# Kernel tuning notes

Hardware: AMD Instinct MI355X
Metric: run time of the kernel (lower is better)

## Reference

```python
import jax, jax.numpy as jnp
import numpy as np

B, S, DIN, DOUT, A, T, H = 8, 1024, 1024, 1024, 4, 4, 8  # arity A, T cell types, hidden H


def setup_inputs() -> dict:
    key = jax.random.key(0)
    ks = jax.random.split(key, 6)
    x = jax.random.normal(ks[0], (B, S, DIN), jnp.float32)
    sc = 1.0 / np.sqrt(DIN).astype(np.float32)
    weight = jax.random.uniform(ks[1], (A * DOUT, DIN), jnp.float32, -sc, sc)
    bias = jax.random.uniform(ks[2], (A * DOUT,), jnp.float32, -sc, sc)
    # stacked per-cell-type MLP params: arity -> H -> 1 (tanh)
    cw1 = jax.random.normal(ks[3], (T, A, H), jnp.float32) / np.sqrt(A).astype(np.float32)
    cb1 = jnp.zeros((T, H), jnp.float32)
    cw2 = jax.random.normal(ks[4], (T, H), jnp.float32) / np.sqrt(H).astype(np.float32)
    cb2 = jnp.zeros((T,), jnp.float32)
    return {"x": x, "weight": weight, "bias": bias,
            "cw1": cw1, "cb1": cb1, "cw2": cw2, "cb2": cb2}


def reference(x, weight, bias, cw1, cb1, cw2, cb2):
    T_, A_, H_ = cw1.shape
    Dout = weight.shape[0] // A_
    G = Dout // T_  # neurons per cell type (cell_indices = contiguous blocks via np.repeat)
    # all_inputs = F.linear(input, weight, bias): (B, S, A*Dout)
    z = jnp.einsum('bsd,od->bso', x, weight) + bias
    # slice per-neuron arity chunks -> (B, S, T, G, A)
    z = z.reshape(z.shape[0], z.shape[1], T_, G, A_)
    # per-cell-type MLP applied to every neuron of that type (replaces Python loop)
    h = jnp.tanh(jnp.einsum('bstga,tah->bstgh', z, cw1) + cb1[:, None, :])
    o = jnp.einsum('bstgh,th->bstg', h, cw2) + cb2[:, None]
    # concat over neurons -> (B, S, Dout)
    return o.reshape(o.shape[0], o.shape[1], Dout)
```

## Files before the change

kernel.cpp:

```cpp
#include <hip/hip_runtime.h>


typedef __bf16 bf16x8 __attribute__((ext_vector_type(8)));
typedef float f32x4 __attribute__((ext_vector_type(4)));
typedef float f32x16 __attribute__((ext_vector_type(16)));

#define BM 256
#define BN 128
#define BK 32
#define KDIM 1024
#define NITER (KDIM / BK)
#define ABUF (BM * BK)
#define BUF_ELEMS ((BM + BN) * BK)
#define BUF_BYTES (BUF_ELEMS * 2)
#define ZS 132
#define XN8 (8192 * 1024 / 8)
#define WN8 (4096 * 1024 / 8)

__global__ __launch_bounds__(256) void cvt_bf16_kernel(
    const float* __restrict__ x, const float* __restrict__ w,
    __bf16* __restrict__ xb, __bf16* __restrict__ wb) {
    int i = blockIdx.x * 256 + threadIdx.x;
    const float* src;
    __bf16* dst;
    int j;
    if (i < XN8) { src = x; dst = xb; j = i; }
    else         { src = w; dst = wb; j = i - XN8; }
    const f32x4* p = (const f32x4*)src + 2 * (size_t)j;
    f32x4 a = p[0], b = p[1];
    bf16x8 o;
    o[0] = (__bf16)a[0]; o[1] = (__bf16)a[1]; o[2] = (__bf16)a[2]; o[3] = (__bf16)a[3];
    o[4] = (__bf16)b[0]; o[5] = (__bf16)b[1]; o[6] = (__bf16)b[2]; o[7] = (__bf16)b[3];
    ((bf16x8*)dst)[j] = o;
}

union __align__(16) SmemU {
    __bf16 stg[2 * BUF_ELEMS];
    float  z[64 * ZS];
};

__global__ __launch_bounds__(256, 2) void fused_gemm_mlp_kernel(
    const __bf16* __restrict__ Ag,
    const __bf16* __restrict__ Bg,
    const float* __restrict__ bias,
    const float* __restrict__ cw1,
    const float* __restrict__ cb1,
    const float* __restrict__ cw2,
    const float* __restrict__ cb2,
    float* __restrict__ out)
{
    __shared__ SmemU u;

    const int tid  = threadIdx.x;
    const int wave = tid >> 6;
    const int lane = tid & 63;
    const int wm = wave >> 1;
    const int wn = wave & 1;
    const int bn0 = blockIdx.x * BN;
    const int bm0 = blockIdx.y * BM;

    f32x16 acc[4][2] = {};

    const int srow4 = lane >> 2;
    const int g8    = (((lane & 3) ^ ((lane >> 3) & 3)) * 8);

    const int lr5 = lane & 31;
    const int lk2 = lane >> 5;
    const int sw2 = (lr5 >> 1) & 3;
    const int arow = (wm * 128 + lr5) * (BK * 2);
    const int brow = ABUF * 2 + (wn * 64 + lr5) * (BK * 2);
    int cxo[2];
#pragma unroll
    for (int kh = 0; kh < 2; ++kh)
        cxo[kh] = ((kh * 2 + lk2) ^ sw2) * 16;
    const char* sb = (const char*)u.stg;

    auto stage = [&](int it, int buf) {
        __bf16* dstA = u.stg + buf * BUF_ELEMS;
        __bf16* dstB = dstA + ABUF;
        const int kof = it * BK;
#pragma unroll
        for (int c = 0; c < 4; ++c) {
            const int chunk = wave * 4 + c;
            const __bf16* ga = Ag + (size_t)(bm0 + chunk * 16 + srow4) * KDIM + kof + g8;
            __builtin_amdgcn_global_load_lds(
                (__attribute__((address_space(1))) void*)ga,
                (__attribute__((address_space(3))) void*)&dstA[chunk * 512],
                16, 0, 0);
        }
#pragma unroll
        for (int c = 0; c < 2; ++c) {
            const int chunk = wave * 2 + c;
            const __bf16* gb = Bg + (size_t)(bn0 + chunk * 16 + srow4) * KDIM + kof + g8;
            __builtin_amdgcn_global_load_lds(
                (__attribute__((address_space(1))) void*)gb,
                (__attribute__((address_space(3))) void*)&dstB[chunk * 512],
                16, 0, 0);
        }
    };

    stage(0, 0);
    for (int it = 0; it < NITER; ++it) {
        __syncthreads();
        if (it + 1 < NITER) stage(it + 1, (it + 1) & 1);
        const char* base = sb + (it & 1) * BUF_BYTES;
#pragma unroll
        for (int kh = 0; kh < 2; ++kh) {
            bf16x8 af[4], bfr[2];
#pragma unroll
            for (int mi = 0; mi < 4; ++mi)
                af[mi] = *(const bf16x8*)(base + arow + mi * 2048 + cxo[kh]);
#pragma unroll
            for (int ni = 0; ni < 2; ++ni)
                bfr[ni] = *(const bf16x8*)(base + brow + ni * 2048 + cxo[kh]);
#pragma unroll
            for (int mi = 0; mi < 4; ++mi)
#pragma unroll
                for (int ni = 0; ni < 2; ++ni)
                    acc[mi][ni] = __builtin_amdgcn_mfma_f32_32x32x16_bf16(
                        af[mi], bfr[ni], acc[mi][ni], 0, 0, 0);
        }
    }
    __syncthreads();

    const int t = bn0 >> 10;
    const float L2E2 = 2.885390081777927f;
    float w1s[32], b1s[8], w2m[8];
#pragma unroll
    for (int i = 0; i < 32; ++i) w1s[i] = cw1[t * 32 + i] * L2E2;
    float oinit = cb2[t];
#pragma unroll
    for (int i = 0; i < 8; ++i) {
        b1s[i] = cb1[t * 8 + i] * L2E2;
        w2m[i] = -2.0f * cw2[t * 8 + i];
        oinit += cw2[t * 8 + i];
    }

    float bcol[2];
#pragma unroll
    for (int ni = 0; ni < 2; ++ni)
        bcol[ni] = bias[bn0 + wn * 64 + ni * 32 + lr5];

#pragma unroll
    for (int h = 0; h < 4; ++h) {
        if (wm == (h >> 1)) {
#pragma unroll
            for (int dmi = 0; dmi < 2; ++dmi) {
                const int mi = (h & 1) * 2 + dmi;
#pragma unroll
                for (int ni = 0; ni < 2; ++ni) {
                    const int n = wn * 64 + ni * 32 + lr5;
#pragma unroll
                    for (int g = 0; g < 4; ++g) {
                        const int rb = dmi * 32 + g * 8 + lk2 * 4;
                        u.z[(rb + 0) * ZS + n] = acc[mi][ni][g * 4 + 0] + bcol[ni];
                        u.z[(rb + 1) * ZS + n] = acc[mi][ni][g * 4 + 1] + bcol[ni];
                        u.z[(rb + 2) * ZS + n] = acc[mi][ni][g * 4 + 2] + bcol[ni];
                        u.z[(rb + 3) * ZS + n] = acc[mi][ni][g * 4 + 3] + bcol[ni];
                    }
                }
            }
        }
        __syncthreads();

#pragma unroll
        for (int it2 = 0; it2 < 8; ++it2) {
            const int i = tid + it2 * 256;
            const int q = i & 31;
            const int r = i >> 5;
            f32x4 z = *(const f32x4*)&u.z[r * ZS + 4 * q];
            float o = oinit;
#pragma unroll
            for (int hh = 0; hh < 8; ++hh) {
                float pre = z[0] * w1s[0 * 8 + hh] + z[1] * w1s[1 * 8 + hh]
                          + z[2] * w1s[2 * 8 + hh] + z[3] * w1s[3 * 8 + hh] + b1s[hh];
                float e = __builtin_amdgcn_exp2f(pre);
                o += w2m[hh] * __builtin_amdgcn_rcpf(e + 1.0f);
            }
            out[(size_t)(bm0 + h * 64 + r) * 1024 + (bn0 >> 2) + q] = o;
        }
        __syncthreads();
    }
}

extern "C" void kernel_launch(void* const* d_in, const int* in_sizes, int n_in,
                              void* d_out, int out_size, void* d_ws, size_t ws_size,
                              hipStream_t stream) {
    const float* x    = (const float*)d_in[0];
    const float* w    = (const float*)d_in[1];
    const float* bias = (const float*)d_in[2];
    const float* cw1  = (const float*)d_in[3];
    const float* cb1  = (const float*)d_in[4];
    const float* cw2  = (const float*)d_in[5];
    const float* cb2  = (const float*)d_in[6];
    float* out = (float*)d_out;

    __bf16* xb = (__bf16*)d_ws;
    __bf16* wb = xb + (size_t)8192 * 1024;

    cvt_bf16_kernel<<<(XN8 + WN8) / 256, 256, 0, stream>>>(x, w, xb, wb);

    dim3 grid(4096 / BN, 8192 / BM);
    fused_gemm_mlp_kernel<<<grid, 256, 0, stream>>>(xb, wb, bias, cw1, cb1, cw2, cb2, out);
}
```

Baseline: 189.7 us.

## Halve M tile, raise occupancy, and use a rotated LDS layout for the epilogue

Shrinks the GEMM tile from 256x128 to 128x128, which halves the accumulator registers, and raises launch bounds to 4 blocks per CU for more occupancy and a larger grid. The MLP weights are now read from global memory (likely scalar loads) instead of being kept in per-thread register arrays. The epilogue staging buffer loses its padding and uses a chunk-rotation swizzle to avoid LDS bank conflicts. The smaller tile gives less operand reuse per block and more total global and L2 traffic.

Result: slower. 200.9 us (+5.9%).

```diff
diff --git a/kernel.cpp b/kernel.cpp
--- a/kernel.cpp
+++ b/kernel.cpp
@@ -5,15 +5,14 @@
 typedef float f32x4 __attribute__((ext_vector_type(4)));
 typedef float f32x16 __attribute__((ext_vector_type(16)));
 
-#define BM 256
+#define BM 128
 #define BN 128
 #define BK 32
 #define KDIM 1024
 #define NITER (KDIM / BK)
-#define ABUF (BM * BK)
-#define BUF_ELEMS ((BM + BN) * BK)
-#define BUF_BYTES (BUF_ELEMS * 2)
-#define ZS 132
+#define ABUF_E (BM * BK)
+#define BUF_E ((BM + BN) * BK)
+#define BUF_BYTES (BUF_E * 2)
 #define XN8 (8192 * 1024 / 8)
 #define WN8 (4096 * 1024 / 8)
 
@@ -35,11 +34,11 @@
 }
 
 union __align__(16) SmemU {
-    __bf16 stg[2 * BUF_ELEMS];
-    float  z[64 * ZS];
+    __bf16 stg[2 * BUF_E];
+    float  z[64 * 128];
 };
 
-__global__ __launch_bounds__(256, 2) void fused_gemm_mlp_kernel(
+__global__ __launch_bounds__(256, 4) void fused_gemm_mlp_kernel(
     const __bf16* __restrict__ Ag,
     const __bf16* __restrict__ Bg,
     const float* __restrict__ bias,
@@ -59,7 +58,7 @@
     const int bn0 = blockIdx.x * BN;
     const int bm0 = blockIdx.y * BM;
 
-    f32x16 acc[4][2] = {};
+    f32x16 acc[2][2] = {};
 
     const int srow4 = lane >> 2;
     const int g8    = (((lane & 3) ^ ((lane >> 3) & 3)) * 8);
@@ -67,33 +66,30 @@
     const int lr5 = lane & 31;
     const int lk2 = lane >> 5;
     const int sw2 = (lr5 >> 1) & 3;
-    const int arow = (wm * 128 + lr5) * (BK * 2);
-    const int brow = ABUF * 2 + (wn * 64 + lr5) * (BK * 2);
+    const int arow = (wm * 64 + lr5) * (BK * 2);
+    const int brow = ABUF_E * 2 + (wn * 64 + lr5) * (BK * 2);
     int cxo[2];
 #pragma unroll
     for (int kh = 0; kh < 2; ++kh)
         cxo[kh] = ((kh * 2 + lk2) ^ sw2) * 16;
     const char* sb = (const char*)u.stg;
 
+    const __bf16* aBase = Ag + (size_t)(bm0 + (wave * 2) * 16 + srow4) * KDIM + g8;
+    const __bf16* bBase = Bg + (size_t)(bn0 + (wave * 2) * 16 + srow4) * KDIM + g8;
+
     auto stage = [&](int it, int buf) {
-        __bf16* dstA = u.stg + buf * BUF_ELEMS;
-        __bf16* dstB = dstA + ABUF;
+        __bf16* dstA = u.stg + buf * BUF_E;
+        __bf16* dstB = dstA + ABUF_E;
         const int kof = it * BK;
-#pragma unroll
-        for (int c = 0; c < 4; ++c) {
-            const int chunk = wave * 4 + c;
-            const __bf16* ga = Ag + (size_t)(bm0 + chunk * 16 + srow4) * KDIM + kof + g8;
-            __builtin_amdgcn_global_load_lds(
-                (__attribute__((address_space(1))) void*)ga,
-                (__attribute__((address_space(3))) void*)&dstA[chunk * 512],
-                16, 0, 0);
-        }
 #pragma unroll
         for (int c = 0; c < 2; ++c) {
             const int chunk = wave * 2 + c;
-            const __bf16* gb = Bg + (size_t)(bn0 + chunk * 16 + srow4) * KDIM + kof + g8;
             __builtin_amdgcn_global_load_lds(
-                (__attribute__((address_space(1))) void*)gb,
+                (__attribute__((address_space(1))) void*)(aBase + (size_t)c * 16 * KDIM + kof),
+                (__attribute__((address_space(3))) void*)&dstA[chunk * 512],
+                16, 0, 0);
+            __builtin_amdgcn_global_load_lds(
+                (__attribute__((address_space(1))) void*)(bBase + (size_t)c * 16 * KDIM + kof),
                 (__attribute__((address_space(3))) void*)&dstB[chunk * 512],
                 16, 0, 0);
         }
@@ -106,15 +102,15 @@
         const char* base = sb + (it & 1) * BUF_BYTES;
 #pragma unroll
         for (int kh = 0; kh < 2; ++kh) {
-            bf16x8 af[4], bfr[2];
+            bf16x8 af[2], bfr[2];
 #pragma unroll
-            for (int mi = 0; mi < 4; ++mi)
+            for (int mi = 0; mi < 2; ++mi)
                 af[mi] = *(const bf16x8*)(base + arow + mi * 2048 + cxo[kh]);
 #pragma unroll
             for (int ni = 0; ni < 2; ++ni)
                 bfr[ni] = *(const bf16x8*)(base + brow + ni * 2048 + cxo[kh]);
 #pragma unroll
-            for (int mi = 0; mi < 4; ++mi)
+            for (int mi = 0; mi < 2; ++mi)
 #pragma unroll
                 for (int ni = 0; ni < 2; ++ni)
                     acc[mi][ni] = __builtin_amdgcn_mfma_f32_32x32x16_bf16(
@@ -125,16 +121,9 @@
 
     const int t = bn0 >> 10;
     const float L2E2 = 2.885390081777927f;
-    float w1s[32], b1s[8], w2m[8];
-#pragma unroll
-    for (int i = 0; i < 32; ++i) w1s[i] = cw1[t * 32 + i] * L2E2;
     float oinit = cb2[t];
 #pragma unroll
-    for (int i = 0; i < 8; ++i) {
-        b1s[i] = cb1[t * 8 + i] * L2E2;
-        w2m[i] = -2.0f * cw2[t * 8 + i];
-        oinit += cw2[t * 8 + i];
-    }
+    for (int i = 0; i < 8; ++i) oinit += cw2[t * 8 + i];
 
     float bcol[2];
 #pragma unroll
@@ -142,21 +131,24 @@
         bcol[ni] = bias[bn0 + wn * 64 + ni * 32 + lr5];
 
 #pragma unroll
-    for (int h = 0; h < 4; ++h) {
-        if (wm == (h >> 1)) {
+    for (int h = 0; h < 2; ++h) {
+        if (wm == h) {
 #pragma unroll
-            for (int dmi = 0; dmi < 2; ++dmi) {
-                const int mi = (h & 1) * 2 + dmi;
+            for (int mi = 0; mi < 2; ++mi) {
 #pragma unroll
                 for (int ni = 0; ni < 2; ++ni) {
-                    const int n = wn * 64 + ni * 32 + lr5;
+                    const int n  = wn * 64 + ni * 32 + lr5;
+                    const int gc = n >> 2;
+                    const int a  = n & 3;
 #pragma unroll
                     for (int g = 0; g < 4; ++g) {
-                        const int rb = dmi * 32 + g * 8 + lk2 * 4;
-                        u.z[(rb + 0) * ZS + n] = acc[mi][ni][g * 4 + 0] + bcol[ni];
-                        u.z[(rb + 1) * ZS + n] = acc[mi][ni][g * 4 + 1] + bcol[ni];
-                        u.z[(rb + 2) * ZS + n] = acc[mi][ni][g * 4 + 2] + bcol[ni];
-                        u.z[(rb + 3) * ZS + n] = acc[mi][ni][g * 4 + 3] + bcol[ni];
+                        const int rb = mi * 32 + g * 8 + lk2 * 4;
+#pragma unroll
+                        for (int j = 0; j < 4; ++j) {
+                            const int chunk = (gc + j) & 31;
+                            u.z[(rb + j) * 128 + chunk * 4 + a] =
+                                acc[mi][ni][g * 4 + j] + bcol[ni];
+                        }
                     }
                 }
             }
@@ -166,16 +158,18 @@
 #pragma unroll
         for (int it2 = 0; it2 < 8; ++it2) {
             const int i = tid + it2 * 256;
-            const int q = i & 31;
-            const int r = i >> 5;
-            f32x4 z = *(const f32x4*)&u.z[r * ZS + 4 * q];
+            const int q = (i & 7) + 8 * ((i >> 8) & 3);
+            const int r = ((i >> 3) & 31) + 32 * (i >> 10);
+            const int chunk = (q + (r & 3)) & 31;
+            f32x4 z = *(const f32x4*)&u.z[r * 128 + chunk * 4];
             float o = oinit;
 #pragma unroll
             for (int hh = 0; hh < 8; ++hh) {
-                float pre = z[0] * w1s[0 * 8 + hh] + z[1] * w1s[1 * 8 + hh]
-                          + z[2] * w1s[2 * 8 + hh] + z[3] * w1s[3 * 8 + hh] + b1s[hh];
-                float e = __builtin_amdgcn_exp2f(pre);
-                o += w2m[hh] * __builtin_amdgcn_rcpf(e + 1.0f);
+                float pre = z[0] * cw1[t * 32 + 0 * 8 + hh] + z[1] * cw1[t * 32 + 1 * 8 + hh]
+                          + z[2] * cw1[t * 32 + 2 * 8 + hh] + z[3] * cw1[t * 32 + 3 * 8 + hh]
+                          + cb1[t * 8 + hh];
+                float e = __builtin_amdgcn_exp2f(pre * L2E2);
+                o -= 2.0f * cw2[t * 8 + hh] * __builtin_amdgcn_rcpf(e + 1.0f);
             }
             out[(size_t)(bm0 + h * 64 + r) * 1024 + (bn0 >> 2) + q] = o;
         }
```
